# Optimization experiments

Measured on AMD Instinct MI355X. Metric: run time of the kernel, lower is better.

The kernel has to match this reference:

```python
import jax, jax.numpy as jnp
import numpy as np

B, C, D, H, W = 4, 256, 16, 16, 16
REDUCTION = 8
CR = C // REDUCTION  # q/k channel dim = 32


def setup_inputs() -> dict:
    key = jax.random.key(0)
    k1, k2, k3, k4, k5, k6 = jax.random.split(key, 6)
    x = jax.random.normal(k1, (B, C, D, H, W), dtype=jnp.float32)
    # 1x1x1 conv weights are just [out_ch, in_ch] matrices
    Wq = jax.random.normal(k2, (CR, C), dtype=jnp.float32) * (1.0 / np.sqrt(C))
    Wk = jax.random.normal(k3, (CR, C), dtype=jnp.float32) * (1.0 / np.sqrt(C))
    Wv = jax.random.normal(k4, (C, C), dtype=jnp.float32) * (1.0 / np.sqrt(C))
    Wo = jax.random.normal(k5, (C, C), dtype=jnp.float32) * (1.0 / np.sqrt(C))
    gamma = jnp.zeros((1,), dtype=jnp.float32) + 0.5  # nonzero so output depends on attention
    return {"x": x, "Wq": Wq, "Wk": Wk, "Wv": Wv, "Wo": Wo, "gamma": gamma}


def reference(x, Wq, Wk, Wv, Wo, gamma):
    b, c, d, h, w = x.shape
    n = d * h * w
    scale = Wq.shape[0] ** -0.5  # (channels // reduction) ** -0.5
    xf = x.reshape(b, c, n)                      # [B, C, N]
    q = jnp.einsum('oc,bcn->bon', Wq, xf)        # [B, CR, N]
    k = jnp.einsum('oc,bcn->bon', Wk, xf)        # [B, CR, N]
    v = jnp.einsum('oc,bcn->bon', Wv, xf)        # [B, C, N]
    attn = jax.nn.softmax(jnp.einsum('bcn,bcm->bnm', q, k) * scale, axis=-1)  # [B, N, N]
    out = jnp.einsum('bcm,bnm->bcn', v, attn)    # v @ attn^T -> [B, C, N]
    out = jnp.einsum('oc,bcn->bon', Wo, out)     # output 1x1x1 conv
    out = out.reshape(b, c, d, h, w)
    return gamma[0] * out + x
```

## Files before the change

### kernel.cpp

```cpp
#include <hip/hip_runtime.h>
#include <hip/hip_bf16.h>

#define BATCH 4
#define CH 256
#define CRD 32
#define NN 4096

typedef __bf16 bf16x8 __attribute__((ext_vector_type(8)));
typedef float floatx4 __attribute__((ext_vector_type(4)));
typedef float floatx16 __attribute__((ext_vector_type(16)));
typedef unsigned short ushort4v __attribute__((ext_vector_type(4)));
typedef unsigned short ushort8v __attribute__((ext_vector_type(8)));

static __device__ __forceinline__ unsigned short f2bf(float f) {
    unsigned int u = __float_as_uint(f);
    u += 0x7fff + ((u >> 16) & 1);
    return (unsigned short)(u >> 16);
}
static __device__ __forceinline__ float bf2f(unsigned short h) {
    return __uint_as_float((unsigned int)h << 16);
}


__global__ __launch_bounds__(256) void wconv_kernel(
    const float* __restrict__ Wq, const float* __restrict__ Wk,
    const float* __restrict__ Wv, const float* __restrict__ Wo,
    unsigned short* __restrict__ What, unsigned short* __restrict__ WobF)
{
    const int o = blockIdx.x;
    const int t = threadIdx.x;
    float scale = 1.0f;
    const float* src;
    if (o < 32)      { src = Wq + o * 256; scale = 0.17677669529663687f; }
    else if (o < 64) { src = Wk + (o - 32) * 256; }
    else             { src = Wv + (o - 64) * 256; }
    const int mb = o >> 5;
    const size_t idx = ((size_t)(mb * 16 + (t >> 4)) * 64
                        + (o & 31) + 32 * ((t >> 3) & 1)) * 8 + (t & 7);
    What[idx] = f2bf(src[t] * scale);
    if (o < 256) {
        const size_t i2 = ((size_t)((o >> 5) * 16 + (t >> 4)) * 64
                           + (o & 31) + 32 * ((t >> 3) & 1)) * 8 + (t & 7);
        WobF[i2] = f2bf(Wo[o * 256 + t]);
    }
}

__global__ __launch_bounds__(256, 2) void qkv_kernel(
    const float* __restrict__ x, const unsigned short* __restrict__ What,
    unsigned short* __restrict__ qh, unsigned short* __restrict__ kh,
    unsigned short* __restrict__ vh)
{
    __shared__ unsigned short xf[16 * 512];

    const int t = threadIdx.x;
    const int w = t >> 6;
    const int l = t & 63;
    const int l31 = l & 31;
    const int h = l >> 5;
    const int nt = blockIdx.x, b = blockIdx.y;
    const int n0 = nt * 32;

    {
        const float* xb = x + (size_t)(b * CH) * NN + n0;
        const int cr = t >> 3;
        const int nc = (t & 7) * 4;
        #pragma unroll
        for (int p = 0; p < 8; ++p) {
            int c = p * 32 + cr;
            floatx4 v4 = *(const floatx4*)(xb + (size_t)c * NN + nc);
            int base = (c >> 4) * 512 + 32 * ((c >> 3) & 1) * 8 + (c & 7);
            xf[base + (nc + 0) * 8] = f2bf(v4[0]);
            xf[base + (nc + 1) * 8] = f2bf(v4[1]);
            xf[base + (nc + 2) * 8] = f2bf(v4[2]);
            xf[base + (nc + 3) * 8] = f2bf(v4[3]);
        }
    }
    __syncthreads();

    const int mb0 = w, mb1 = w + 4, mb2 = w + 8;
    floatx16 acc0, acc1, acc2;
    #pragma unroll
    for (int i = 0; i < 16; ++i) { acc0[i] = 0.f; acc1[i] = 0.f; acc2[i] = 0.f; }

    for (int kblk = 0; kblk < 16; ++kblk) {
        bf16x8 bf = *(const bf16x8*)&xf[kblk * 512 + l * 8];
        bf16x8 a0 = *(const bf16x8*)(What + ((size_t)(mb0 * 16 + kblk) * 64 + l) * 8);
        bf16x8 a1 = *(const bf16x8*)(What + ((size_t)(mb1 * 16 + kblk) * 64 + l) * 8);
        acc0 = __builtin_amdgcn_mfma_f32_32x32x16_bf16(a0, bf, acc0, 0, 0, 0);
        acc1 = __builtin_amdgcn_mfma_f32_32x32x16_bf16(a1, bf, acc1, 0, 0, 0);
        if (w < 2) {
            bf16x8 a2 = *(const bf16x8*)(What + ((size_t)(mb2 * 16 + kblk) * 64 + l) * 8);
            acc2 = __builtin_amdgcn_mfma_f32_32x32x16_bf16(a2, bf, acc2, 0, 0, 0);
        }
    }

    auto store_qk = [&](unsigned short* dst, const floatx16& a) {
        size_t base = (size_t)(b * 128 + nt) * 1024;
        #pragma unroll
        for (int r = 0; r < 16; ++r) {
            int rowo = (r & 3) + 8 * (r >> 2) + 4 * h;
            size_t idx = base + (size_t)(rowo >> 4) * 512
                         + (size_t)(l31 + 32 * ((rowo >> 3) & 1)) * 8 + (rowo & 7);
            dst[idx] = f2bf(a[r]);
        }
    };
    auto store_v = [&](int cblk, const floatx16& a) {
        size_t base = (((size_t)b * 8 + cblk) * 256 + nt * 2 + (l31 >> 4)) * 512
                      + 32 * ((l31 >> 3) & 1) * 8 + (l31 & 7);
        #pragma unroll
        for (int r = 0; r < 16; ++r) {
            int rowo = (r & 3) + 8 * (r >> 2) + 4 * h;
            vh[base + rowo * 8] = f2bf(a[r]);
        }
    };

    if (w == 0)      store_qk(qh, acc0);
    else if (w == 1) store_qk(kh, acc0);
    else             store_v(w - 2, acc0);
    store_v(w + 2, acc1);
    if (w < 2) store_v(w + 6, acc2);
}

__global__ __launch_bounds__(256, 4) void attn_kernel(
    const unsigned short* __restrict__ qh, const unsigned short* __restrict__ kh,
    const unsigned short* __restrict__ vh, unsigned short* __restrict__ Opart,
    float* __restrict__ ml)
{
    __shared__ unsigned short p_lds[8 * 64 * 8];
    __shared__ float pmax_s[4][32];
    __shared__ float psum_s[4][32];

    const int t = threadIdx.x;
    const int w = t >> 6;
    const int l = t & 63;
    const int l31 = l & 31;
    const int h = l >> 5;
    const int g = blockIdx.x, ks = blockIdx.y, b = blockIdx.z;

    const unsigned short* qB = qh + (size_t)(b * 128 + g) * 1024;
    const unsigned short* kB = kh + (size_t)b * 128 * 1024;
    const unsigned short* vB = vh + (size_t)b * 8 * 256 * 512;

    bf16x8 qf0 = *(const bf16x8*)(qB + l * 8);
    bf16x8 qf1 = *(const bf16x8*)(qB + 512 + l * 8);

    bf16x8 kf0 = *(const bf16x8*)(kB + (size_t)(ks * 64 + w) * 1024 + l * 8);
    bf16x8 kf1 = *(const bf16x8*)(kB + (size_t)(ks * 64 + w) * 1024 + 512 + l * 8);

    float m_run = -1e30f, l_run = 0.f;
    floatx16 acc0, acc1;
    #pragma unroll
    for (int i = 0; i < 16; ++i) { acc0[i] = 0.f; acc1[i] = 0.f; }

    for (int it = 0; it < 16; ++it) {
        floatx16 sacc;
        #pragma unroll
        for (int i = 0; i < 16; ++i) sacc[i] = 0.f;
        sacc = __builtin_amdgcn_mfma_f32_32x32x16_bf16(kf0, qf0, sacc, 0, 0, 0);
        sacc = __builtin_amdgcn_mfma_f32_32x32x16_bf16(kf1, qf1, sacc, 0, 0, 0);

        float pm = sacc[0];
        #pragma unroll
        for (int r = 1; r < 16; ++r) pm = fmaxf(pm, sacc[r]);
        pm = fmaxf(pm, __shfl_xor(pm, 32));
        if (h == 0) pmax_s[w][l31] = pm;
        __syncthreads();

        float mnew = fmaxf(fmaxf(pmax_s[0][l31], pmax_s[1][l31]),
                           fmaxf(pmax_s[2][l31], pmax_s[3][l31]));
        mnew = fmaxf(m_run, mnew);
        float alpha = __expf(m_run - mnew);
        m_run = mnew;
        float pv[16];
        float psum = 0.f;
        #pragma unroll
        for (int r = 0; r < 16; ++r) {
            pv[r] = __expf(sacc[r] - mnew);
            psum += pv[r];
        }
        psum += __shfl_xor(psum, 32);
        if (h == 0) psum_s[w][l31] = psum;
        #pragma unroll
        for (int rg = 0; rg < 4; ++rg) {
            ushort4v pk;
            #pragma unroll
            for (int i = 0; i < 4; ++i) pk[i] = f2bf(pv[rg * 4 + i]);
            int idx = ((2 * w + (rg >> 1)) * 64 + l31 + 32 * (rg & 1)) * 8 + 4 * h;
            *(ushort4v*)&p_lds[idx] = pk;
        }
        if (it < 15) {
            const unsigned short* kn = kB + (size_t)(ks * 64 + (it + 1) * 4 + w) * 1024;
            kf0 = *(const bf16x8*)(kn + l * 8);
            kf1 = *(const bf16x8*)(kn + 512 + l * 8);
        }
        __syncthreads();

        float isum = (psum_s[0][l31] + psum_s[1][l31]) +
                     (psum_s[2][l31] + psum_s[3][l31]);
        l_run = l_run * alpha + isum;
        #pragma unroll
        for (int i = 0; i < 16; ++i) { acc0[i] *= alpha; acc1[i] *= alpha; }

        const unsigned short* v0b = vB + ((size_t)(2 * w) * 256 + (ks * 16 + it) * 8) * 512;
        const unsigned short* v1b = vB + ((size_t)(2 * w + 1) * 256 + (ks * 16 + it) * 8) * 512;
        bf16x8 va = *(const bf16x8*)(v0b + l * 8);
        bf16x8 vc = *(const bf16x8*)(v1b + l * 8);
        bf16x8 pf = *(const bf16x8*)&p_lds[l * 8];
        #pragma unroll
        for (int s = 0; s < 8; ++s) {
            bf16x8 va_n, vc_n, pf_n;
            if (s < 7) {
                va_n = *(const bf16x8*)(v0b + (s + 1) * 512 + l * 8);
                vc_n = *(const bf16x8*)(v1b + (s + 1) * 512 + l * 8);
                pf_n = *(const bf16x8*)&p_lds[((s + 1) * 64 + l) * 8];
            }
            acc0 = __builtin_amdgcn_mfma_f32_32x32x16_bf16(va, pf, acc0, 0, 0, 0);
            acc1 = __builtin_amdgcn_mfma_f32_32x32x16_bf16(vc, pf, acc1, 0, 0, 0);
            va = va_n; vc = vc_n; pf = pf_n;
        }
    }

    unsigned short* op = Opart + ((size_t)((b * 128 + g) * 2 + ks)) * 8192;
    #pragma unroll
    for (int ct = 0; ct < 2; ++ct) {
        const floatx16& a = ct ? acc1 : acc0;
        #pragma unroll
        for (int rg = 0; rg < 4; ++rg) {
            ushort4v pk;
            #pragma unroll
            for (int i = 0; i < 4; ++i) pk[i] = f2bf(a[rg * 4 + i]);
            int sP = 4 * w + 2 * ct + (rg >> 1);
            size_t idx = ((size_t)sP * 64 + l31 + 32 * (rg & 1)) * 8 + 4 * h;
            *(ushort4v*)(op + idx) = pk;
        }
    }
    if (w == 0 && h == 0) {
        size_t mb = ((size_t)(b * 128 + g) * 2 + ks) * 64;
        ml[mb + l31] = m_run;
        ml[mb + 32 + l31] = l_run;
    }
}

__global__ __launch_bounds__(256, 2) void out_kernel(
    const unsigned short* __restrict__ Opart, const float* __restrict__ ml,
    const unsigned short* __restrict__ WobF, const float* __restrict__ x,
    const float* __restrict__ gamma, float* __restrict__ out)
{
    const int t = threadIdx.x;
    const int w = t >> 6;
    const int l = t & 63;
    const int l31 = l & 31;
    const int h = l >> 5;
    const int qt = blockIdx.x, b = blockIdx.y;

    const size_t mb = (size_t)(b * 128 + qt) * 2 * 64;
    float m0 = ml[mb + l31],       l0 = ml[mb + 32 + l31];
    float m1 = ml[mb + 64 + l31],  l1 = ml[mb + 96 + l31];
    float M  = fmaxf(m0, m1);
    float e0 = __expf(m0 - M), e1 = __expf(m1 - M);
    float Lc = l0 * e0 + l1 * e1;
    float w0 = e0 / Lc, w1 = e1 / Lc;

    const unsigned short* o0 = Opart + ((size_t)(b * 128 + qt) * 2 + 0) * 8192;
    const unsigned short* o1 = Opart + ((size_t)(b * 128 + qt) * 2 + 1) * 8192;

    floatx16 acc[2];
    #pragma unroll
    for (int m = 0; m < 2; ++m)
        #pragma unroll
        for (int i = 0; i < 16; ++i) acc[m][i] = 0.f;

    for (int s = 0; s < 16; ++s) {
        ushort8v f0 = *(const ushort8v*)(o0 + (s * 64 + l) * 8);
        ushort8v f1 = *(const ushort8v*)(o1 + (s * 64 + l) * 8);
        ushort8v cmb;
        #pragma unroll
        for (int j = 0; j < 8; ++j)
            cmb[j] = f2bf(w0 * bf2f(f0[j]) + w1 * bf2f(f1[j]));
        bf16x8 bfr = *(bf16x8*)&cmb;
        #pragma unroll
        for (int m = 0; m < 2; ++m) {
            int mt = 2 * w + m;
            bf16x8 af = *(const bf16x8*)(WobF + ((size_t)(mt * 16 + s) * 64 + l) * 8);
            acc[m] = __builtin_amdgcn_mfma_f32_32x32x16_bf16(af, bfr, acc[m], 0, 0, 0);
        }
    }

    const float gm = gamma[0];
    #pragma unroll
    for (int m = 0; m < 2; ++m)
        #pragma unroll
        for (int r = 0; r < 16; ++r) {
            int o = (2 * w + m) * 32 + (r & 3) + 8 * (r >> 2) + 4 * h;
            int n = qt * 32 + l31;
            size_t oi = ((size_t)(b * 256 + o)) * NN + n;
            out[oi] = gm * acc[m][r] + x[oi];
        }
}

extern "C" void kernel_launch(void* const* d_in, const int* in_sizes, int n_in,
                              void* d_out, int out_size, void* d_ws, size_t ws_size,
                              hipStream_t stream)
{
    const float* x     = (const float*)d_in[0];
    const float* Wq    = (const float*)d_in[1];
    const float* Wk    = (const float*)d_in[2];
    const float* Wv    = (const float*)d_in[3];
    const float* Wo    = (const float*)d_in[4];
    const float* gamma = (const float*)d_in[5];
    float* out = (float*)d_out;

    char* wsb = (char*)d_ws;
    unsigned short* qh    = (unsigned short*)(wsb);
    unsigned short* kh    = (unsigned short*)(wsb + (1u << 20));
    unsigned short* vh    = (unsigned short*)(wsb + (2u << 20));
    unsigned short* What  = (unsigned short*)(wsb + (10u << 20));
    unsigned short* WobF  = (unsigned short*)(wsb + (10u << 20) + (256u << 10));
    unsigned short* Opart = (unsigned short*)(wsb + (11u << 20));
    float*          ml    = (float*)         (wsb + (28u << 20));

    wconv_kernel<<<320, 256, 0, stream>>>(Wq, Wk, Wv, Wo, What, WobF);

    dim3 g1(128, BATCH);
    qkv_kernel<<<g1, 256, 0, stream>>>(x, What, qh, kh, vh);

    dim3 g2(128, 2, BATCH);
    attn_kernel<<<g2, 256, 0, stream>>>(qh, kh, vh, Opart, ml);

    dim3 g3(128, BATCH);
    out_kernel<<<g3, 256, 0, stream>>>(Opart, ml, WobF, x, gamma, out);
}
```

Before: 164.7 us.

## Split attention key range four ways and vectorize qkv LDS and stores

The attention kernel now splits the key dimension into four chunks instead of two, doubling the grid to 2048 blocks and raising the occupancy hint, so more blocks are available to fill the GPU. The output kernel merges four partial softmax results instead of two. The qkv kernel also loads x with coalesced per-column reads and writes packed 4-element vectors to LDS and to the q/k outputs, replacing scalar scatter stores. In exchange, the partial-output buffer and the merge traffic in the output kernel double, and the larger launch-bounds hint may force register spills.

New measurement: 223.1 us. 35.5% more time.

```diff
diff --git a/kernel.cpp b/kernel.cpp
--- a/kernel.cpp
+++ b/kernel.cpp
@@ -62,17 +62,20 @@
 
     {
         const float* xb = x + (size_t)(b * CH) * NN + n0;
-        const int cr = t >> 3;
-        const int nc = (t & 7) * 4;
+        const int n = t & 31;
+        const int cq = t >> 5;
         #pragma unroll
         for (int p = 0; p < 8; ++p) {
-            int c = p * 32 + cr;
-            floatx4 v4 = *(const floatx4*)(xb + (size_t)c * NN + nc);
-            int base = (c >> 4) * 512 + 32 * ((c >> 3) & 1) * 8 + (c & 7);
-            xf[base + (nc + 0) * 8] = f2bf(v4[0]);
-            xf[base + (nc + 1) * 8] = f2bf(v4[1]);
-            xf[base + (nc + 2) * 8] = f2bf(v4[2]);
-            xf[base + (nc + 3) * 8] = f2bf(v4[3]);
+            int c = p * 32 + cq * 4;
+            float v0 = xb[(size_t)(c + 0) * NN + n];
+            float v1 = xb[(size_t)(c + 1) * NN + n];
+            float v2 = xb[(size_t)(c + 2) * NN + n];
+            float v3 = xb[(size_t)(c + 3) * NN + n];
+            ushort4v u4;
+            u4[0] = f2bf(v0); u4[1] = f2bf(v1); u4[2] = f2bf(v2); u4[3] = f2bf(v3);
+            int addr = ((2 * p + (cq >> 2)) * 64 + n + 32 * ((cq >> 1) & 1)) * 8
+                       + 4 * (cq & 1);
+            *(ushort4v*)&xf[addr] = u4;
         }
     }
     __syncthreads();
@@ -97,11 +100,13 @@
     auto store_qk = [&](unsigned short* dst, const floatx16& a) {
         size_t base = (size_t)(b * 128 + nt) * 1024;
         #pragma unroll
-        for (int r = 0; r < 16; ++r) {
-            int rowo = (r & 3) + 8 * (r >> 2) + 4 * h;
-            size_t idx = base + (size_t)(rowo >> 4) * 512
-                         + (size_t)(l31 + 32 * ((rowo >> 3) & 1)) * 8 + (rowo & 7);
-            dst[idx] = f2bf(a[r]);
+        for (int rg = 0; rg < 4; ++rg) {
+            ushort4v u4;
+            #pragma unroll
+            for (int i = 0; i < 4; ++i) u4[i] = f2bf(a[rg * 4 + i]);
+            size_t idx = base + (size_t)(rg >> 1) * 512
+                         + (size_t)(l31 + 32 * (rg & 1)) * 8 + 4 * h;
+            *(ushort4v*)(dst + idx) = u4;
         }
     };
     auto store_v = [&](int cblk, const floatx16& a) {
@@ -121,7 +126,7 @@
     if (w < 2) store_v(w + 6, acc2);
 }
 
-__global__ __launch_bounds__(256, 4) void attn_kernel(
+__global__ __launch_bounds__(256, 8) void attn_kernel(
     const unsigned short* __restrict__ qh, const unsigned short* __restrict__ kh,
     const unsigned short* __restrict__ vh, unsigned short* __restrict__ Opart,
     float* __restrict__ ml)
@@ -144,15 +149,15 @@
     bf16x8 qf0 = *(const bf16x8*)(qB + l * 8);
     bf16x8 qf1 = *(const bf16x8*)(qB + 512 + l * 8);
 
-    bf16x8 kf0 = *(const bf16x8*)(kB + (size_t)(ks * 64 + w) * 1024 + l * 8);
-    bf16x8 kf1 = *(const bf16x8*)(kB + (size_t)(ks * 64 + w) * 1024 + 512 + l * 8);
+    bf16x8 kf0 = *(const bf16x8*)(kB + (size_t)(ks * 32 + w) * 1024 + l * 8);
+    bf16x8 kf1 = *(const bf16x8*)(kB + (size_t)(ks * 32 + w) * 1024 + 512 + l * 8);
 
     float m_run = -1e30f, l_run = 0.f;
     floatx16 acc0, acc1;
     #pragma unroll
     for (int i = 0; i < 16; ++i) { acc0[i] = 0.f; acc1[i] = 0.f; }
 
-    for (int it = 0; it < 16; ++it) {
+    for (int it = 0; it < 8; ++it) {
         floatx16 sacc;
         #pragma unroll
         for (int i = 0; i < 16; ++i) sacc[i] = 0.f;
@@ -188,8 +193,8 @@
             int idx = ((2 * w + (rg >> 1)) * 64 + l31 + 32 * (rg & 1)) * 8 + 4 * h;
             *(ushort4v*)&p_lds[idx] = pk;
         }
-        if (it < 15) {
-            const unsigned short* kn = kB + (size_t)(ks * 64 + (it + 1) * 4 + w) * 1024;
+        if (it < 7) {
+            const unsigned short* kn = kB + (size_t)(ks * 32 + (it + 1) * 4 + w) * 1024;
             kf0 = *(const bf16x8*)(kn + l * 8);
             kf1 = *(const bf16x8*)(kn + 512 + l * 8);
         }
@@ -201,8 +206,8 @@
         #pragma unroll
         for (int i = 0; i < 16; ++i) { acc0[i] *= alpha; acc1[i] *= alpha; }
 
-        const unsigned short* v0b = vB + ((size_t)(2 * w) * 256 + (ks * 16 + it) * 8) * 512;
-        const unsigned short* v1b = vB + ((size_t)(2 * w + 1) * 256 + (ks * 16 + it) * 8) * 512;
+        const unsigned short* v0b = vB + ((size_t)(2 * w) * 256 + (ks * 8 + it) * 8) * 512;
+        const unsigned short* v1b = vB + ((size_t)(2 * w + 1) * 256 + (ks * 8 + it) * 8) * 512;
         bf16x8 va = *(const bf16x8*)(v0b + l * 8);
         bf16x8 vc = *(const bf16x8*)(v1b + l * 8);
         bf16x8 pf = *(const bf16x8*)&p_lds[l * 8];
@@ -220,7 +225,7 @@
         }
     }
 
-    unsigned short* op = Opart + ((size_t)((b * 128 + g) * 2 + ks)) * 8192;
+    unsigned short* op = Opart + ((size_t)((b * 128 + g) * 4 + ks)) * 8192;
     #pragma unroll
     for (int ct = 0; ct < 2; ++ct) {
         const floatx16& a = ct ? acc1 : acc0;
@@ -235,7 +240,7 @@
         }
     }
     if (w == 0 && h == 0) {
-        size_t mb = ((size_t)(b * 128 + g) * 2 + ks) * 64;
+        size_t mb = ((size_t)(b * 128 + g) * 4 + ks) * 64;
         ml[mb + l31] = m_run;
         ml[mb + 32 + l31] = l_run;
     }
@@ -253,16 +258,21 @@
     const int h = l >> 5;
     const int qt = blockIdx.x, b = blockIdx.y;
 
-    const size_t mb = (size_t)(b * 128 + qt) * 2 * 64;
-    float m0 = ml[mb + l31],       l0 = ml[mb + 32 + l31];
-    float m1 = ml[mb + 64 + l31],  l1 = ml[mb + 96 + l31];
-    float M  = fmaxf(m0, m1);
+    const size_t slot = (size_t)(b * 128 + qt) * 4;
+    float m0 = ml[(slot + 0) * 64 + l31], l0 = ml[(slot + 0) * 64 + 32 + l31];
+    float m1 = ml[(slot + 1) * 64 + l31], l1 = ml[(slot + 1) * 64 + 32 + l31];
+    float m2 = ml[(slot + 2) * 64 + l31], l2 = ml[(slot + 2) * 64 + 32 + l31];
+    float m3 = ml[(slot + 3) * 64 + l31], l3 = ml[(slot + 3) * 64 + 32 + l31];
+    float M = fmaxf(fmaxf(m0, m1), fmaxf(m2, m3));
     float e0 = __expf(m0 - M), e1 = __expf(m1 - M);
-    float Lc = l0 * e0 + l1 * e1;
-    float w0 = e0 / Lc, w1 = e1 / Lc;
-
-    const unsigned short* o0 = Opart + ((size_t)(b * 128 + qt) * 2 + 0) * 8192;
-    const unsigned short* o1 = Opart + ((size_t)(b * 128 + qt) * 2 + 1) * 8192;
+    float e2 = __expf(m2 - M), e3 = __expf(m3 - M);
+    float Lc = l0 * e0 + l1 * e1 + l2 * e2 + l3 * e3;
+    float w0 = e0 / Lc, w1 = e1 / Lc, w2 = e2 / Lc, w3 = e3 / Lc;
+
+    const unsigned short* o0 = Opart + (slot + 0) * 8192;
+    const unsigned short* o1 = Opart + (slot + 1) * 8192;
+    const unsigned short* o2 = Opart + (slot + 2) * 8192;
+    const unsigned short* o3 = Opart + (slot + 3) * 8192;
 
     floatx16 acc[2];
     #pragma unroll
@@ -273,10 +283,13 @@
     for (int s = 0; s < 16; ++s) {
         ushort8v f0 = *(const ushort8v*)(o0 + (s * 64 + l) * 8);
         ushort8v f1 = *(const ushort8v*)(o1 + (s * 64 + l) * 8);
+        ushort8v f2 = *(const ushort8v*)(o2 + (s * 64 + l) * 8);
+        ushort8v f3 = *(const ushort8v*)(o3 + (s * 64 + l) * 8);
         ushort8v cmb;
         #pragma unroll
         for (int j = 0; j < 8; ++j)
-            cmb[j] = f2bf(w0 * bf2f(f0[j]) + w1 * bf2f(f1[j]));
+            cmb[j] = f2bf(w0 * bf2f(f0[j]) + w1 * bf2f(f1[j])
+                        + w2 * bf2f(f2[j]) + w3 * bf2f(f3[j]));
         bf16x8 bfr = *(bf16x8*)&cmb;
         #pragma unroll
         for (int m = 0; m < 2; ++m) {
@@ -317,14 +330,14 @@
     unsigned short* What  = (unsigned short*)(wsb + (10u << 20));
     unsigned short* WobF  = (unsigned short*)(wsb + (10u << 20) + (256u << 10));
     unsigned short* Opart = (unsigned short*)(wsb + (11u << 20));
-    float*          ml    = (float*)         (wsb + (28u << 20));
+    float*          ml    = (float*)         (wsb + (45u << 20));
 
     wconv_kernel<<<320, 256, 0, stream>>>(Wq, Wk, Wv, Wo, What, WobF);
 
     dim3 g1(128, BATCH);
     qkv_kernel<<<g1, 256, 0, stream>>>(x, What, qh, kh, vh);
 
-    dim3 g2(128, 2, BATCH);
+    dim3 g2(128, 4, BATCH);
     attn_kernel<<<g2, 256, 0, stream>>>(qh, kh, vh, Opart, ml);
 
     dim3 g3(128, BATCH);
```
